# Performance work log

Measured on AMD Instinct MI355X. Metric: run time of the kernel, lower is better.

## Reference

```python
import jax, jax.numpy as jnp
import numpy as np

B, S, D, H = 2, 2048, 2048, 16
HD = D // H


def setup_inputs() -> dict:
    key = jax.random.key(0)
    kx, = jax.random.split(key, 1)
    return {
        "x": jax.random.normal(kx, (B, S, D), dtype=jnp.float32),
        "q_mask": jnp.ones((D, D), dtype=jnp.float32),
        "k_mask": jnp.ones((D, D), dtype=jnp.float32),
        "v_mask": jnp.ones((D, D), dtype=jnp.float32),
        "out_mask": jnp.ones((D, D), dtype=jnp.float32),
        "head_mask": jnp.ones((H,), dtype=jnp.float32),
        "attention_mask": jnp.ones((B, S), dtype=jnp.float32),
        "shared_weight": jnp.float32(1.0),
    }


def reference(x, q_mask, k_mask, v_mask, out_mask, head_mask, attention_mask, shared_weight):
    b, s, d = x.shape
    scale = jnp.float32(HD) ** -0.5

    def shared_linear(inp, mask):
        # F.linear(x, mask * shared_weight): out = inp @ (mask*sw).T
        return jnp.einsum("bsd,ed->bse", inp, mask * shared_weight)

    q = shared_linear(x, q_mask).reshape(b, s, H, HD).transpose(0, 2, 1, 3)  # [B,H,S,HD]
    k = shared_linear(x, k_mask).reshape(b, s, H, HD).transpose(0, 2, 1, 3)
    v = shared_linear(x, v_mask).reshape(b, s, H, HD).transpose(0, 2, 1, 3)

    hm = head_mask.reshape(1, H, 1, 1)
    q, k, v = q * hm, k * hm, v * hm

    scores = jnp.einsum("bhqd,bhkd->bhqk", q, k) * scale  # [B,H,S,S]

    # causal mask: upper triangle (j > i) -> -inf
    causal = jnp.triu(jnp.ones((s, s), dtype=bool), k=1)
    scores = jnp.where(causal, -jnp.inf, scores)

    # additive attention mask: (1 - m) * -10000, broadcast [B,1,1,S]
    scores = scores + (1.0 - attention_mask)[:, None, None, :] * -10000.0

    attn = jax.nn.softmax(scores, axis=-1)  # dropout is identity in eval / p=0

    out = jnp.einsum("bhqk,bhkd->bhqd", attn, v)          # [B,H,S,HD]
    out = out.transpose(0, 2, 1, 3).reshape(b, s, d)       # [B,S,D]
    return shared_linear(out, out_mask)
```

## Files before the change

### kernel.cpp

```cpp
#include <hip/hip_runtime.h>

#define B_  2
#define S_  2048
#define D_  2048
#define H_  16
#define HD_ 128

typedef __bf16 bf16;
typedef __bf16 bf16x4 __attribute__((ext_vector_type(4)));
typedef __bf16 bf16x8 __attribute__((ext_vector_type(8)));
typedef float  f32x4  __attribute__((ext_vector_type(4)));
typedef unsigned int u32x4 __attribute__((ext_vector_type(4)));

__device__ __forceinline__ void gld_lds16(const void* g, void* l) {
    __builtin_amdgcn_global_load_lds(
        (const __attribute__((address_space(1))) unsigned int*)g,
        (__attribute__((address_space(3))) unsigned int*)l, 16, 0, 0);
}

__device__ __forceinline__ f32x4 mfma16(bf16x8 a, bf16x8 b, f32x4 c) {
    return __builtin_amdgcn_mfma_f32_16x16x32_bf16(a, b, c, 0, 0, 0);
}

#define BAR()  asm volatile("s_barrier" ::: "memory")
#define WAIT_LGKM0() do { asm volatile("s_waitcnt lgkmcnt(0)" ::: "memory"); \
                          __builtin_amdgcn_sched_barrier(0); } while (0)

__global__ __launch_bounds__(256)
void precast_all(const float* __restrict__ x, bf16* __restrict__ xh,
                 bf16* __restrict__ xl,
                 const float* __restrict__ qm, bf16* __restrict__ qmb,
                 const float* __restrict__ km, bf16* __restrict__ kmb,
                 const float* __restrict__ swp) {
    int bid = blockIdx.x;
    if (bid < 4096) {
        int i = (bid * 256 + threadIdx.x) * 8;
        float4 a = *(const float4*)(x + i);
        float4 b = *(const float4*)(x + i + 4);
        float av[8] = {a.x, a.y, a.z, a.w, b.x, b.y, b.z, b.w};
        bf16x8 h8, l8;
#pragma unroll
        for (int e = 0; e < 8; e++) {
            bf16 hv = (bf16)av[e];
            h8[e] = hv;
            l8[e] = (bf16)(av[e] - (float)hv);
        }
        *(bf16x8*)(xh + i) = h8;
        *(bf16x8*)(xl + i) = l8;
        return;
    }
    const float sw = swp[0];
    bid -= 4096;
    const float* src = qm; bf16* dst = qmb;
    if (bid >= 2048) { src = km; dst = kmb; bid -= 2048; }
    int i = (bid * 256 + threadIdx.x) * 8;
    float4 a = *(const float4*)(src + i);
    float4 b = *(const float4*)(src + i + 4);
    bf16x8 o;
    o[0] = (bf16)(a.x * sw); o[1] = (bf16)(a.y * sw);
    o[2] = (bf16)(a.z * sw); o[3] = (bf16)(a.w * sw);
    o[4] = (bf16)(b.x * sw); o[5] = (bf16)(b.y * sw);
    o[6] = (bf16)(b.z * sw); o[7] = (bf16)(b.w * sw);
    *(bf16x8*)(dst + i) = o;
}

__global__ __launch_bounds__(256)
void precast_mask(const float* __restrict__ s0, bf16* __restrict__ d0,
                  const float* __restrict__ swp) {
    const float sw = swp[0];
    int i = (blockIdx.x * 256 + threadIdx.x) * 8;
    float4 a = *(const float4*)(s0 + i);
    float4 b = *(const float4*)(s0 + i + 4);
    bf16x8 o;
    o[0] = (bf16)(a.x * sw); o[1] = (bf16)(a.y * sw);
    o[2] = (bf16)(a.z * sw); o[3] = (bf16)(a.w * sw);
    o[4] = (bf16)(b.x * sw); o[5] = (bf16)(b.y * sw);
    o[6] = (bf16)(b.z * sw); o[7] = (bf16)(b.w * sw);
    *(bf16x8*)(d0 + i) = o;
}

template<int BM, int BN, int MODE>
__global__ __launch_bounds__(256, 2)
void gemm2p(const bf16* __restrict__ Ah_g, const bf16* __restrict__ Al_g,
            const bf16* __restrict__ Bq, const bf16* __restrict__ Bk,
            const float* __restrict__ hm,
            bf16* __restrict__ o_qh, bf16* __restrict__ o_ql,
            bf16* __restrict__ o_kh, bf16* __restrict__ o_kl,
            bf16* __restrict__ o_vt, float* __restrict__ o_f32,
            int nt) {
    constexpr int IM = BM / 2 / 16;
    constexpr int JN = BN / 2 / 16;
    constexpr int IH = IM / 2;
    constexpr int ISSA = BM / 64;
    constexpr int ISSB = BN / 64;
    constexpr int BUFE = (BM + BN) * 32;
    constexpr int SMELEMS = (MODE == 1 && BN * (BM + 8) > 2 * BUFE)
                                ? BN * (BM + 8) : 2 * BUFE;
    __shared__ bf16 sm[SMELEMS];

    const int t = threadIdx.x;
    const int wave = t >> 6, lane = t & 63;
    const int lrow = lane & 15, quad = lane >> 4;
    const int wr = wave >> 1, wc = wave & 1;

    const int gx = gridDim.x;
    const int id0 = blockIdx.y * gx + blockIdx.x;
    const int nwg = gx * gridDim.y;
    const int id = (id0 & 7) * (nwg >> 3) + (id0 >> 3);
    const int m0 = (id / gx) * BM, n0 = (id % gx) * BN;

    const int nsec = (MODE == 0) ? (n0 & (D_ - 1)) : n0;
    const bf16* Bg = (MODE == 0 && n0 >= D_) ? Bk : Bq;

    const int arow = wr * (BM / 2) + lrow;
    const int brow = wc * (BN / 2) + lrow;
    const int gsw = (quad ^ ((lrow >> 1) & 3)) * 8;

    const int srr = lane >> 2, spg = lane & 3;
    const int ssw = (spg ^ ((srr >> 1) & 3)) * 8;

    auto stage_A = [&](int kt, int pbuf) {
        const bf16* As = (MODE == 0 && kt >= 64) ? Al_g : Ah_g;
        const int kc = ((MODE == 0) ? (kt & 63) : kt) * 32;
        bf16* buf = sm + pbuf * BUFE;
#pragma unroll
        for (int pp = 0; pp < ISSA; pp++) {
            int r0 = wave * (BM / 4) + pp * 16;
            gld_lds16(As + (size_t)(m0 + r0 + srr) * D_ + kc + ssw,
                      buf + r0 * 32);
        }
    };
    auto stage_B = [&](int kt, int pbuf) {
        const int kc = ((MODE == 0) ? (kt & 63) : kt) * 32;
        bf16* buf = sm + pbuf * BUFE + BM * 32;
#pragma unroll
        for (int pp = 0; pp < ISSB; pp++) {
            int r0 = wave * (BN / 4) + pp * 16;
            gld_lds16(Bg + (size_t)(nsec + r0 + srr) * D_ + kc + ssw,
                      buf + r0 * 32);
        }
    };

    f32x4 acc[IM][JN];
#pragma unroll
    for (int i = 0; i < IM; i++)
#pragma unroll
        for (int j = 0; j < JN; j++) acc[i][j] = (f32x4){0.f, 0.f, 0.f, 0.f};

    stage_A(0, 0); stage_B(0, 0); stage_B(1, 1);

    int p = 0;
    for (int kt = 0; kt < nt; ++kt) {
        if (kt < nt - 1) asm volatile("s_waitcnt vmcnt(2)" ::: "memory");
        else             asm volatile("s_waitcnt vmcnt(0)" ::: "memory");
        BAR();
        if (kt + 1 < nt) stage_A(kt + 1, p ^ 1);

        const bf16* Ab = sm + p * BUFE;
        const bf16* Bb = Ab + BM * 32;
        bf16x8 a[IH], b[JN];

#pragma unroll
        for (int j = 0; j < JN; j++)
            b[j] = *(const bf16x8*)&Bb[(brow + j * 16) * 32 + gsw];
#pragma unroll
        for (int i = 0; i < IH; i++)
            a[i] = *(const bf16x8*)&Ab[(arow + i * 16) * 32 + gsw];
        BAR();
        WAIT_LGKM0();
        __builtin_amdgcn_s_setprio(1);
#pragma unroll
        for (int i = 0; i < IH; i++)
#pragma unroll
            for (int j = 0; j < JN; j++)
                acc[i][j] = mfma16(a[i], b[j], acc[i][j]);
        __builtin_amdgcn_s_setprio(0);
        BAR();

        if (kt + 2 < nt) stage_B(kt + 2, p);

#pragma unroll
        for (int i = 0; i < IH; i++)
            a[i] = *(const bf16x8*)&Ab[(arow + (IH + i) * 16) * 32 + gsw];
        WAIT_LGKM0();
        __builtin_amdgcn_s_setprio(1);
#pragma unroll
        for (int i = 0; i < IH; i++)
#pragma unroll
            for (int j = 0; j < JN; j++)
                acc[IH + i][j] = mfma16(a[i], b[j], acc[IH + i][j]);
        __builtin_amdgcn_s_setprio(0);
        p ^= 1;
    }

    if constexpr (MODE == 0) {
        const bool isq = (n0 < D_);
        bf16* oh = isq ? o_qh : o_kh;
        bf16* ol = isq ? o_ql : o_kl;
#pragma unroll
        for (int j = 0; j < JN; j++) {
            int nb = nsec + wc * (BN / 2) + j * 16;
            int h = nb >> 7;
            float hv = hm[h];
#pragma unroll
            for (int i = 0; i < IM; i++) {
                int mB = m0 + wr * (BM / 2) + i * 16 + quad * 4;
                int bb = mB >> 11, s = mB & (S_ - 1);
                size_t idx0 = (((size_t)bb * H_ + h) * S_ + s) * HD_ + (nb & 127) + lrow;
#pragma unroll
                for (int r = 0; r < 4; r++) {
                    float v = acc[i][j][r] * hv;
                    bf16 hvv = (bf16)v;
                    bf16 lvv = (bf16)(v - (float)hvv);
                    oh[idx0 + (size_t)r * HD_] = hvv;
                    ol[idx0 + (size_t)r * HD_] = lvv;
                }
            }
        }
    }
    if constexpr (MODE == 1) {
        __syncthreads();
        bf16* tr = sm;
#pragma unroll
        for (int j = 0; j < JN; j++) {
            int nl = wc * (BN / 2) + j * 16 + lrow;
            float hv = hm[(n0 + nl) >> 7];
#pragma unroll
            for (int i = 0; i < IM; i++) {
                int ml = wr * (BM / 2) + i * 16 + quad * 4;
                bf16x4 pk;
#pragma unroll
                for (int r = 0; r < 4; r++) pk[r] = (bf16)(acc[i][j][r] * hv);
                *(bf16x4*)&tr[nl * 136 + ml] = pk;
            }
        }
        __syncthreads();
        const int bI = m0 >> 11;
        const int s0 = m0 & (S_ - 1);
#pragma unroll
        for (int w = 0; w < 8; w++) {
            int nrow = w * 16 + (t >> 4);
            int c = t & 15;
            bf16x8 vv = *(const bf16x8*)&tr[nrow * 136 + c * 8];
            int ng = n0 + nrow;
            int h = ng >> 7, hd = ng & 127;
            *(bf16x8*)&o_vt[((size_t)(bI * H_ + h) * HD_ + hd) * S_ + s0 + c * 8] = vv;
        }
    }
    if constexpr (MODE == 2) {
#pragma unroll
        for (int j = 0; j < JN; j++) {
            int n = n0 + wc * (BN / 2) + j * 16 + lrow;
#pragma unroll
            for (int i = 0; i < IM; i++) {
                int mB = m0 + wr * (BM / 2) + i * 16 + quad * 4;
#pragma unroll
                for (int r = 0; r < 4; r++)
                    o_f32[(size_t)(mB + r) * D_ + n] = acc[i][j][r];
            }
        }
    }
}

#define SPLD 72

__global__ __launch_bounds__(256, 2)
void attn_kernel(const bf16* __restrict__ qh_, const bf16* __restrict__ ql_,
                 const bf16* __restrict__ kh_, const bf16* __restrict__ kl_,
                 const bf16* __restrict__ vt_, const float* __restrict__ am,
                 bf16* __restrict__ outp) {
    const int id = blockIdx.x;
    const int xcd = id & 7, slot = id >> 3;
    const int bh = xcd * 4 + (slot & 3);
    const int qblk = 31 - (slot >> 2);
    const int b = bh >> 4, h = bh & 15;
    const int i0 = qblk * 64;
    const int t = threadIdx.x, wave = t >> 6, lane = t & 63;
    const int lrow = lane & 15, quad = lane >> 4;

    __shared__ bf16 skh[64 * 128];
    __shared__ bf16 skl[64 * 128];
    __shared__ bf16 svt[128 * 64];
    __shared__ bf16 sp[4][16 * SPLD];
    __shared__ float samadd[S_];

    const size_t kbase = (size_t)bh * S_ * HD_;
    const size_t vbase = (size_t)bh * HD_ * S_;

    {
        int j = t * 8;
        float4 a0 = *(const float4*)(am + b * S_ + j);
        float4 a1 = *(const float4*)(am + b * S_ + j + 4);
        float4 r0 = {(1.0f - a0.x) * -10000.0f, (1.0f - a0.y) * -10000.0f,
                     (1.0f - a0.z) * -10000.0f, (1.0f - a0.w) * -10000.0f};
        float4 r1 = {(1.0f - a1.x) * -10000.0f, (1.0f - a1.y) * -10000.0f,
                     (1.0f - a1.z) * -10000.0f, (1.0f - a1.w) * -10000.0f};
        *(float4*)&samadd[j] = r0;
        *(float4*)&samadd[j + 4] = r1;
    }

    const int qrow = i0 + wave * 16 + lrow;
    bf16x8 qhf[4], qlf[4];
#pragma unroll
    for (int c = 0; c < 4; c++) {
        qhf[c] = *(const bf16x8*)&qh_[kbase + (size_t)qrow * HD_ + c * 32 + quad * 8];
        qlf[c] = *(const bf16x8*)&ql_[kbase + (size_t)qrow * HD_ + c * 32 + quad * 8];
    }

    u32x4 kpre[8], vpre[4];
    auto issueKV = [&](int j0) {
#pragma unroll
        for (int p = 0; p < 4; p++) {
            int rb = wave * 16 + p * 4;
            int r = rb + (lane >> 4);
            int gl = ((lane & 15) ^ (r & 7)) * 8;
            kpre[p]     = *(const u32x4*)(kh_ + kbase + (size_t)(j0 + r) * HD_ + gl);
            kpre[4 + p] = *(const u32x4*)(kl_ + kbase + (size_t)(j0 + r) * HD_ + gl);
        }
#pragma unroll
        for (int p = 0; p < 4; p++) {
            int db = wave * 32 + p * 8;
            int d = db + (lane >> 3);
            int gl = ((lane & 7) ^ (d & 7)) * 8;
            vpre[p] = *(const u32x4*)(vt_ + vbase + (size_t)d * S_ + j0 + gl);
        }
    };
    auto writeKV = [&]() {
#pragma unroll
        for (int p = 0; p < 4; p++) {
            int rb = wave * 16 + p * 4;
            *(u32x4*)&skh[rb * 128 + lane * 8] = kpre[p];
            *(u32x4*)&skl[rb * 128 + lane * 8] = kpre[4 + p];
        }
#pragma unroll
        for (int p = 0; p < 4; p++) {
            int db = wave * 32 + p * 8;
            *(u32x4*)&svt[db * 64 + lane * 8] = vpre[p];
        }
    };

    float m_i[4], l_i[4];
    f32x4 O[8];
#pragma unroll
    for (int r = 0; r < 4; r++) { m_i[r] = -INFINITY; l_i[r] = 0.f; }
#pragma unroll
    for (int n2 = 0; n2 < 8; n2++) O[n2] = (f32x4){0.f, 0.f, 0.f, 0.f};

    const float scale = 0.08838834764831845f;

    issueKV(0);
    __syncthreads();

    for (int j0 = 0; j0 <= i0; j0 += 64) {
        BAR();
        writeKV();
        if (j0 + 64 <= i0) issueKV(j0 + 64);
        asm volatile("s_waitcnt lgkmcnt(0)" ::: "memory");
        BAR();

        float amadd[4];
#pragma unroll
        for (int nt = 0; nt < 4; nt++)
            amadd[nt] = samadd[j0 + nt * 16 + lrow];

        f32x4 s4[4];
#pragma unroll
        for (int nt = 0; nt < 4; nt++) s4[nt] = (f32x4){0.f, 0.f, 0.f, 0.f};
        __builtin_amdgcn_s_setprio(1);
#pragma unroll
        for (int c = 0; c < 4; c++) {
#pragma unroll
            for (int nt = 0; nt < 4; nt++) {
                int ka = (nt * 16 + lrow) * 128 + (((c * 4 + quad) ^ (lrow & 7)) * 8);
                bf16x8 kb8 = *(const bf16x8*)&skh[ka];
                bf16x8 lb8 = *(const bf16x8*)&skl[ka];
                s4[nt] = mfma16(qhf[c], kb8, s4[nt]);
                s4[nt] = mfma16(qhf[c], lb8, s4[nt]);
                s4[nt] = mfma16(qlf[c], kb8, s4[nt]);
            }
        }
        __builtin_amdgcn_s_setprio(0);

        const bool diag = (j0 == i0);
#pragma unroll
        for (int r = 0; r < 4; r++) {
            const int rrow = wave * 16 + quad * 4 + r;
            float sv[4], pw[4];
            float mx = -INFINITY;
#pragma unroll
            for (int nt = 0; nt < 4; nt++) {
                float xv = s4[nt][r] * scale + amadd[nt];
                if (diag && (nt * 16 + lrow) > rrow) xv = -INFINITY;
                sv[nt] = xv;
                mx = fmaxf(mx, xv);
            }
#pragma unroll
            for (int off = 1; off < 16; off <<= 1) mx = fmaxf(mx, __shfl_xor(mx, off));
            float mnew = fmaxf(m_i[r], mx);
            float alpha = __expf(m_i[r] - mnew);
            float ps = 0.f;
#pragma unroll
            for (int nt = 0; nt < 4; nt++) { pw[nt] = __expf(sv[nt] - mnew); ps += pw[nt]; }
#pragma unroll
            for (int off = 1; off < 16; off <<= 1) ps += __shfl_xor(ps, off);
            l_i[r] = l_i[r] * alpha + ps;
            m_i[r] = mnew;
#pragma unroll
            for (int n2 = 0; n2 < 8; n2++) O[n2][r] *= alpha;
#pragma unroll
            for (int nt = 0; nt < 4; nt++)
                sp[wave][(quad * 4 + r) * SPLD + nt * 16 + lrow] = (bf16)pw[nt];
        }
        asm volatile("s_waitcnt lgkmcnt(0)" ::: "memory");

        __builtin_amdgcn_s_setprio(1);
#pragma unroll
        for (int k2 = 0; k2 < 2; k2++) {
            bf16x8 pf = *(const bf16x8*)&sp[wave][lrow * SPLD + k2 * 32 + quad * 8];
            const int gp = ((quad + k2 * 4) ^ (lrow & 7)) * 8;
#pragma unroll
            for (int n2 = 0; n2 < 8; n2++) {
                bf16x8 vf8 = *(const bf16x8*)&svt[(n2 * 16 + lrow) * 64 + gp];
                O[n2] = mfma16(pf, vf8, O[n2]);
            }
        }
        __builtin_amdgcn_s_setprio(0);
    }

    float inv[4];
#pragma unroll
    for (int r = 0; r < 4; r++) inv[r] = 1.0f / l_i[r];
#pragma unroll
    for (int n2 = 0; n2 < 8; n2++)
#pragma unroll
        for (int r = 0; r < 4; r++) {
            int srow = i0 + wave * 16 + quad * 4 + r;
            outp[((size_t)(b * S_ + srow)) * D_ + h * HD_ + n2 * 16 + lrow] =
                (bf16)(O[n2][r] * inv[r]);
        }
}

extern "C" void kernel_launch(void* const* d_in, const int* in_sizes, int n_in,
                              void* d_out, int out_size, void* d_ws, size_t ws_size,
                              hipStream_t stream) {
    const float* x  = (const float*)d_in[0];
    const float* qm = (const float*)d_in[1];
    const float* km = (const float*)d_in[2];
    const float* vm = (const float*)d_in[3];
    const float* om = (const float*)d_in[4];
    const float* hm = (const float*)d_in[5];
    const float* am = (const float*)d_in[6];
    const float* sw = (const float*)d_in[7];
    float* out = (float*)d_out;

    const size_t P = (size_t)B_ * H_ * S_ * HD_ * sizeof(bf16);
    char* ws = (char*)d_ws;
    bf16* xh = (bf16*)(ws + 0 * P);
    bf16* xl = (bf16*)(ws + 1 * P);
    bf16* qh = (bf16*)(ws + 2 * P);
    bf16* ql = (bf16*)(ws + 3 * P);
    bf16* kh = (bf16*)(ws + 4 * P);
    bf16* kl = (bf16*)(ws + 5 * P);
    bf16* attn_out = xh;
    bf16* vmb = xl;
    bf16* omb = qh;
    bf16* vt  = (bf16*)d_out;
    bf16* qmb = (bf16*)((char*)d_out + 16u * 1024 * 1024);
    bf16* kmb = (bf16*)((char*)d_out + 24u * 1024 * 1024);

    precast_all<<<8192, 256, 0, stream>>>(x, xh, xl, qm, qmb, km, kmb, sw);

    gemm2p<256, 128, 0><<<dim3(32, 16), 256, 0, stream>>>(
        xh, xl, qmb, kmb, hm, qh, ql, kh, kl, nullptr, nullptr, 128);

    precast_mask<<<2048, 256, 0, stream>>>(vm, vmb, sw);
    gemm2p<128, 128, 1><<<dim3(16, 32), 256, 0, stream>>>(
        xh, nullptr, vmb, nullptr, hm,
        nullptr, nullptr, nullptr, nullptr, vt, nullptr, 64);

    attn_kernel<<<1024, 256, 0, stream>>>(qh, ql, kh, kl, vt, am, attn_out);

    precast_mask<<<2048, 256, 0, stream>>>(om, omb, sw);
    gemm2p<128, 128, 2><<<dim3(16, 32), 256, 0, stream>>>(
        attn_out, nullptr, omb, nullptr, hm,
        nullptr, nullptr, nullptr, nullptr, nullptr, out, 64);
}
```

Measured before the change: 488.4 us.

## Add 256x256 eight-wave QK projection GEMM with quadrant-staged LDS pipeline

Replaces the Q/K projection GEMM with a new 512-thread kernel using 256x256 output tiles and a 64-wide K step. It stages A/B halves into LDS in a staggered double-buffered schedule interleaved with four quadrant MFMA phases, and remaps blocks across XCDs. The goal is more data reuse per LDS load and better overlap of global loads with compute. It also removes a barrier and LDS waits in the remaining gemm2p loop, which risks reading LDS before the loads complete and relies on the compiler inserting waits.

```diff
diff --git a/kernel.cpp b/kernel.cpp
--- a/kernel.cpp
+++ b/kernel.cpp
@@ -77,6 +77,166 @@
     o[4] = (bf16)(b.x * sw); o[5] = (bf16)(b.y * sw);
     o[6] = (bf16)(b.z * sw); o[7] = (bf16)(b.w * sw);
     *(bf16x8*)(d0 + i) = o;
+}
+
+__global__ __launch_bounds__(512, 1)
+void gemm8x(const bf16* __restrict__ Ah_g, const bf16* __restrict__ Al_g,
+            const bf16* __restrict__ Bq, const bf16* __restrict__ Bk,
+            const float* __restrict__ hm,
+            bf16* __restrict__ o_qh, bf16* __restrict__ o_ql,
+            bf16* __restrict__ o_kh, bf16* __restrict__ o_kl,
+            int nt) {
+    __shared__ bf16 sm[2 * 4 * 128 * 64];
+    const int t = threadIdx.x;
+    const int wave = t >> 6, lane = t & 63;
+    const int lrow = lane & 15, quad = lane >> 4;
+    const int wr = wave >> 2, wc = wave & 3;
+
+    const int gx = gridDim.x;
+    const int id0 = blockIdx.y * gx + blockIdx.x;
+    const int id = (id0 & 7) * 32 + (id0 >> 3);
+    const int m0 = (id / gx) * 256, n0 = (id % gx) * 256;
+
+    const int nsec = n0 & (D_ - 1);
+    const bf16* Bg = (n0 >= D_) ? Bk : Bq;
+
+    const int g0 = (quad ^ (lrow & 7)) * 8;
+    const int g1 = ((4 + quad) ^ (lrow & 7)) * 8;
+
+    auto stage_half = [&](int kt, int p, int h) {
+        if (kt >= nt) return;
+        const bf16* plane = (kt >= 32) ? Al_g : Ah_g;
+        const int kc = (kt & 31) * 64;
+        bf16* dst = sm + (p * 4 + h) * (128 * 64);
+#pragma unroll
+        for (int is = 0; is < 2; is++) {
+            int rbase = wave * 16 + is * 8;
+            int r = rbase + (lane >> 3);
+            int gsrc = ((lane & 7) ^ (r & 7)) * 8;
+            const bf16* g = (h < 2)
+                ? plane + (size_t)(m0 + h * 128 + r) * D_ + kc + gsrc
+                : Bg + (size_t)(nsec + (h - 2) * 128 + r) * D_ + kc + gsrc;
+            gld_lds16(g, dst + rbase * 64);
+        }
+    };
+    auto rdAq = [&](int p, int qm, int i, int ge) -> bf16x8 {
+        const bf16* base = sm + (p * 4 + wr) * (128 * 64);
+        return *(const bf16x8*)&base[(qm * 64 + i * 16 + lrow) * 64 + ge];
+    };
+    auto rdBq = [&](int p, int qn, int j, int ge) -> bf16x8 {
+        const bf16* base = sm + (p * 4 + 2 + (wc >> 1)) * (128 * 64);
+        return *(const bf16x8*)&base[((wc & 1) * 64 + qn * 32 + j * 16 + lrow) * 64 + ge];
+    };
+
+    f32x4 acc[8][4];
+#pragma unroll
+    for (int i = 0; i < 8; i++)
+#pragma unroll
+        for (int j = 0; j < 4; j++) acc[i][j] = (f32x4){0.f, 0.f, 0.f, 0.f};
+
+    bf16x8 aF[4][2], bQ0[2][2], bQ1[2][2];
+
+    auto quadmm = [&](int qm, int qn, bf16x8 (&a)[4][2], bf16x8 (&b)[2][2]) {
+        __builtin_amdgcn_s_setprio(1);
+#pragma unroll
+        for (int i = 0; i < 4; i++)
+#pragma unroll
+            for (int j = 0; j < 2; j++) {
+                acc[qm * 4 + i][qn * 2 + j] =
+                    mfma16(a[i][0], b[j][0], acc[qm * 4 + i][qn * 2 + j]);
+                acc[qm * 4 + i][qn * 2 + j] =
+                    mfma16(a[i][1], b[j][1], acc[qm * 4 + i][qn * 2 + j]);
+            }
+        __builtin_amdgcn_s_setprio(0);
+    };
+
+    stage_half(0, 0, 0); stage_half(0, 0, 1); stage_half(0, 0, 2); stage_half(0, 0, 3);
+    stage_half(1, 1, 2); stage_half(1, 1, 3);
+    asm volatile("s_waitcnt vmcnt(4)" ::: "memory");
+    BAR();
+
+    const int nj = nt >> 1;
+    for (int J = 0; J < nj; ++J) {
+        const int tq = 2 * J;
+        const bool last = (J == nj - 1);
+
+#pragma unroll
+        for (int i = 0; i < 4; i++) { aF[i][0] = rdAq(0, 0, i, g0); aF[i][1] = rdAq(0, 0, i, g1); }
+#pragma unroll
+        for (int j = 0; j < 2; j++) { bQ0[j][0] = rdBq(0, 0, j, g0); bQ0[j][1] = rdBq(0, 0, j, g1); }
+        stage_half(tq + 1, 1, 0);
+        BAR(); WAIT_LGKM0();
+        quadmm(0, 0, aF, bQ0);
+        BAR();
+#pragma unroll
+        for (int j = 0; j < 2; j++) { bQ1[j][0] = rdBq(0, 1, j, g0); bQ1[j][1] = rdBq(0, 1, j, g1); }
+        stage_half(tq + 1, 1, 1);
+        BAR(); WAIT_LGKM0();
+        quadmm(0, 1, aF, bQ1);
+        BAR();
+#pragma unroll
+        for (int i = 0; i < 4; i++) { aF[i][0] = rdAq(0, 1, i, g0); aF[i][1] = rdAq(0, 1, i, g1); }
+        stage_half(tq + 2, 0, 2);
+        BAR(); WAIT_LGKM0();
+        quadmm(1, 0, aF, bQ0);
+        BAR();
+        stage_half(tq + 2, 0, 3);
+        if (last) asm volatile("s_waitcnt vmcnt(0)" ::: "memory");
+        else      asm volatile("s_waitcnt vmcnt(4)" ::: "memory");
+        BAR();
+        quadmm(1, 1, aF, bQ1);
+        BAR();
+#pragma unroll
+        for (int i = 0; i < 4; i++) { aF[i][0] = rdAq(1, 0, i, g0); aF[i][1] = rdAq(1, 0, i, g1); }
+#pragma unroll
+        for (int j = 0; j < 2; j++) { bQ0[j][0] = rdBq(1, 0, j, g0); bQ0[j][1] = rdBq(1, 0, j, g1); }
+        stage_half(tq + 2, 0, 0);
+        BAR(); WAIT_LGKM0();
+        quadmm(0, 0, aF, bQ0);
+        BAR();
+#pragma unroll
+        for (int j = 0; j < 2; j++) { bQ1[j][0] = rdBq(1, 1, j, g0); bQ1[j][1] = rdBq(1, 1, j, g1); }
+        stage_half(tq + 2, 0, 1);
+        BAR(); WAIT_LGKM0();
+        quadmm(0, 1, aF, bQ1);
+        BAR();
+#pragma unroll
+        for (int i = 0; i < 4; i++) { aF[i][0] = rdAq(1, 1, i, g0); aF[i][1] = rdAq(1, 1, i, g1); }
+        stage_half(tq + 3, 1, 2);
+        BAR(); WAIT_LGKM0();
+        quadmm(1, 0, aF, bQ0);
+        BAR();
+        stage_half(tq + 3, 1, 3);
+        if (last) asm volatile("s_waitcnt vmcnt(0)" ::: "memory");
+        else      asm volatile("s_waitcnt vmcnt(4)" ::: "memory");
+        BAR();
+        quadmm(1, 1, aF, bQ1);
+        BAR();
+    }
+
+    const bool isq = (n0 < D_);
+    bf16* oh = isq ? o_qh : o_kh;
+    bf16* ol = isq ? o_ql : o_kl;
+#pragma unroll
+    for (int j = 0; j < 4; j++) {
+        int nb = nsec + wc * 64 + j * 16;
+        int h = nb >> 7;
+        float hv = hm[h];
+#pragma unroll
+        for (int i = 0; i < 8; i++) {
+            int mB = m0 + wr * 128 + i * 16 + quad * 4;
+            int bb = mB >> 11, s = mB & (S_ - 1);
+            size_t idx0 = (((size_t)bb * H_ + h) * S_ + s) * HD_ + (nb & 127) + lrow;
+#pragma unroll
+            for (int r = 0; r < 4; r++) {
+                float v = acc[i][j][r] * hv;
+                bf16 hvv = (bf16)v;
+                bf16 lvv = (bf16)(v - (float)hvv);
+                oh[idx0 + (size_t)r * HD_] = hvv;
+                ol[idx0 + (size_t)r * HD_] = lvv;
+            }
+        }
+    }
 }
 
 template<int BM, int BN, int MODE>
@@ -166,8 +326,6 @@
 #pragma unroll
         for (int i = 0; i < IH; i++)
             a[i] = *(const bf16x8*)&Ab[(arow + i * 16) * 32 + gsw];
-        BAR();
-        WAIT_LGKM0();
         __builtin_amdgcn_s_setprio(1);
 #pragma unroll
         for (int i = 0; i < IH; i++)
@@ -182,7 +340,6 @@
 #pragma unroll
         for (int i = 0; i < IH; i++)
             a[i] = *(const bf16x8*)&Ab[(arow + (IH + i) * 16) * 32 + gsw];
-        WAIT_LGKM0();
         __builtin_amdgcn_s_setprio(1);
 #pragma unroll
         for (int i = 0; i < IH; i++)
@@ -470,8 +627,8 @@
 
     precast_all<<<8192, 256, 0, stream>>>(x, xh, xl, qm, qmb, km, kmb, sw);
 
-    gemm2p<256, 128, 0><<<dim3(32, 16), 256, 0, stream>>>(
-        xh, xl, qmb, kmb, hm, qh, ql, kh, kl, nullptr, nullptr, 128);
+    gemm8x<<<dim3(16, 16), 512, 0, stream>>>(
+        xh, xl, qmb, kmb, hm, qh, ql, kh, kl, 64);
 
     precast_mask<<<2048, 256, 0, stream>>>(vm, vmb, sw);
     gemm2p<128, 128, 1><<<dim3(16, 32), 256, 0, stream>>>(
```

New measurement: 495.2 us. No clear change (+1.4%).
